# Kernel optimization log

Measured on AMD Instinct MI355X. Metric: run time of the kernel, lower is better.

## Reference

```python
import jax, jax.numpy as jnp
import numpy as np

N = 10000          # num nodes
E = 640000         # num edges (avg degree 64)
IN_CH = 128
OUT_CH = 128


def setup_inputs() -> dict:
    key = jax.random.key(0)
    k_x, k_ei, k_ea, k_w1, k_b1, k_w2, k_b2 = jax.random.split(key, 7)
    x = jax.random.normal(k_x, (N, IN_CH), dtype=jnp.float32)
    edge_index = jax.random.randint(k_ei, (2, E), 0, N, dtype=jnp.int64)
    edge_attr = jax.random.uniform(k_ea, (E,), dtype=jnp.float32)
    # MLP params: Linear(2*in, out) -> ReLU -> Linear(out, out), stored as [in, out]
    s1 = 1.0 / np.sqrt(2 * IN_CH)
    s2 = 1.0 / np.sqrt(OUT_CH)
    W1 = jax.random.uniform(k_w1, (2 * IN_CH, OUT_CH), jnp.float32, -s1, s1)
    b1 = jax.random.uniform(k_b1, (OUT_CH,), jnp.float32, -s1, s1)
    W2 = jax.random.uniform(k_w2, (OUT_CH, OUT_CH), jnp.float32, -s2, s2)
    b2 = jax.random.uniform(k_b2, (OUT_CH,), jnp.float32, -s2, s2)
    return {"x": x, "edge_index": edge_index, "edge_attr": edge_attr,
            "W1": W1, "b1": b1, "W2": W2, "b2": b2}


def reference(x, edge_index, edge_attr, W1, b1, W2, b2):
    row, col = edge_index[0], edge_index[1]
    # message: scale sender feature by edge_attr, concat with receiver feature, 2-layer MLP
    x_i = x[row] * edge_attr[:, None]          # [E, in]
    x_j = x[col]                               # [E, in]
    combined = jnp.concatenate([x_i, x_j], axis=1)  # [E, 2*in]
    h = jax.nn.relu(combined @ W1 + b1)        # [E, out]
    messages = h @ W2 + b2                     # [E, out]
    # sum aggregation: scatter-add messages into receiving nodes (col)
    out = jnp.zeros((x.shape[0], messages.shape[1]), dtype=messages.dtype)
    out = out.at[col].add(messages)
    return out
```

## Files before the change

kernel.cpp:

```cpp
#include <hip/hip_runtime.h>

#define C 128
#define NPB 16
#define NSLAB 8
#define CAP8 24
#define OVF_MAX 65536
#define EPT 8

__device__ __forceinline__ unsigned bf16_bits(float x) {
    unsigned u = __float_as_uint(x);
    u += 0x7FFFu + ((u >> 16) & 1u);
    return u >> 16;
}
__device__ __forceinline__ float bf16f(unsigned short b) {
    return __uint_as_float(((unsigned)b) << 16);
}

__global__ void fused_pre_kernel(const float* __restrict__ x, const float* __restrict__ W1,
                                 unsigned short* __restrict__ P16, float* __restrict__ Q,
                                 const int* __restrict__ ei, const float* __restrict__ attr,
                                 int* __restrict__ cursor, int* __restrict__ ovf_cnt,
                                 int2* __restrict__ ovf, unsigned* __restrict__ sorted,
                                 int N, int E, int SB) {
    if ((int)blockIdx.x < SB) {
        const int slab = blockIdx.x & (NSLAB - 1);
        int* __restrict__ cur = cursor + (size_t)slab * N;
        unsigned* __restrict__ sl = sorted + (size_t)slab * N * CAP8;
        const int base = (blockIdx.x * 256 + threadIdx.x) * EPT;
        if (base >= E) return;
        if (base + EPT <= E) {
            const int4 r0 = *(const int4*)(ei + base);
            const int4 r1 = *(const int4*)(ei + base + 4);
            const int4 c0 = *(const int4*)(ei + (size_t)E + base);
            const int4 c1 = *(const int4*)(ei + (size_t)E + base + 4);
            const float4 a0 = *(const float4*)(attr + base);
            const float4 a1 = *(const float4*)(attr + base + 4);
            const int rows[EPT] = {r0.x, r0.y, r0.z, r0.w, r1.x, r1.y, r1.z, r1.w};
            const int cols[EPT] = {c0.x, c0.y, c0.z, c0.w, c1.x, c1.y, c1.z, c1.w};
            const float as[EPT] = {a0.x, a0.y, a0.z, a0.w, a1.x, a1.y, a1.z, a1.w};
            int pos[EPT];
#pragma unroll
            for (int j = 0; j < EPT; ++j)
                pos[j] = atomicAdd(&cur[cols[j]], 1);
#pragma unroll
            for (int j = 0; j < EPT; ++j) {
                const unsigned v = (bf16_bits(as[j]) << 16) | (unsigned)rows[j];
                if (pos[j] < CAP8) {
                    sl[(size_t)cols[j] * CAP8 + pos[j]] = v;
                } else {
                    const int o = atomicAdd(ovf_cnt, 1);
                    if (o < OVF_MAX) ovf[o] = make_int2(cols[j], (int)v);
                }
            }
        } else {
            for (int e = base; e < E; ++e) {
                const int row = ei[e], colv = ei[(size_t)E + e];
                const int pos = atomicAdd(&cur[colv], 1);
                const unsigned v = (bf16_bits(attr[e]) << 16) | (unsigned)row;
                if (pos < CAP8) sl[(size_t)colv * CAP8 + pos] = v;
                else {
                    const int o = atomicAdd(ovf_cnt, 1);
                    if (o < OVF_MAX) ovf[o] = make_int2(colv, (int)v);
                }
            }
        }
    } else {
        __shared__ float xs[NPB][C];
        const int pb = blockIdx.x - SB;
        const int n0 = pb * NPB;
        const int tt = threadIdx.x & (C - 1);
        const int half = threadIdx.x >> 7;
        for (int i = threadIdx.x; i < NPB * C; i += 256) {
            const int gi = n0 * C + i;
            xs[0][i] = (gi < N * C) ? x[gi] : 0.f;
        }
        __syncthreads();
        const float* __restrict__ Wb = W1 + (half ? (C * C) : 0) + tt;
        float acc[NPB] = {};
        for (int k = 0; k < C; ++k) {
            const float w = Wb[k * C];
#pragma unroll
            for (int j = 0; j < NPB; ++j)
                acc[j] = fmaf(xs[j][k], w, acc[j]);
        }
#pragma unroll
        for (int j = 0; j < NPB; ++j)
            if (n0 + j < N) {
                if (half) Q[(size_t)(n0 + j) * C + tt] = acc[j];
                else      P16[(size_t)(n0 + j) * C + tt] = (unsigned short)bf16_bits(acc[j]);
            }
    }
}

__global__ void agg_out_kernel(const unsigned* __restrict__ sorted, const int* __restrict__ cursor,
                               const unsigned short* __restrict__ P16, const float* __restrict__ Q,
                               const float* __restrict__ b1, const float* __restrict__ W2,
                               const float* __restrict__ b2,
                               const int* __restrict__ ovf_cnt, const int2* __restrict__ ovf,
                               float* __restrict__ out, int N) {
    __shared__ float4 part[2][4][32];
    __shared__ float hs[2][C];
    const int t = threadIdx.x;
    const int j = t >> 7;
    const int slice = (t >> 5) & 3;
    const int ch4 = t & 31;
    const int n = blockIdx.x * 2 + j;

    float4 acc = make_float4(0.f, 0.f, 0.f, 0.f);
    float4 qb = acc;
    int deg = 0;
    if (n < N) {
        int cnts[NSLAB];
#pragma unroll
        for (int s = 0; s < NSLAB; ++s) {
            cnts[s] = cursor[(size_t)s * N + n];
            deg += cnts[s];
        }
        const float4 q4  = *(const float4*)(Q + (size_t)n * C + (ch4 << 2));
        const float4 b14 = *(const float4*)(b1 + (ch4 << 2));
        qb = make_float4(q4.x + b14.x, q4.y + b14.y, q4.z + b14.z, q4.w + b14.w);
#pragma unroll
        for (int si = 0; si < 2; ++si) {
            const int s = slice + (si << 2);
            const int cs = min(cnts[s], CAP8);
            const unsigned* __restrict__ buf = sorted + ((size_t)s * N + n) * CAP8;
            int i = 0;
            for (; i + 4 <= cs; i += 4) {
                const uint4 v = *(const uint4*)(buf + i);
                const ushort4 p0 = *(const ushort4*)(P16 + (((size_t)(v.x & 0xFFFFu)) << 7) + (ch4 << 2));
                const ushort4 p1 = *(const ushort4*)(P16 + (((size_t)(v.y & 0xFFFFu)) << 7) + (ch4 << 2));
                const ushort4 p2 = *(const ushort4*)(P16 + (((size_t)(v.z & 0xFFFFu)) << 7) + (ch4 << 2));
                const ushort4 p3 = *(const ushort4*)(P16 + (((size_t)(v.w & 0xFFFFu)) << 7) + (ch4 << 2));
                const float a0 = __uint_as_float(v.x & 0xFFFF0000u);
                const float a1 = __uint_as_float(v.y & 0xFFFF0000u);
                const float a2 = __uint_as_float(v.z & 0xFFFF0000u);
                const float a3 = __uint_as_float(v.w & 0xFFFF0000u);
                acc.x += fmaxf(fmaf(a0, bf16f(p0.x), qb.x), 0.f) + fmaxf(fmaf(a1, bf16f(p1.x), qb.x), 0.f)
                       + fmaxf(fmaf(a2, bf16f(p2.x), qb.x), 0.f) + fmaxf(fmaf(a3, bf16f(p3.x), qb.x), 0.f);
                acc.y += fmaxf(fmaf(a0, bf16f(p0.y), qb.y), 0.f) + fmaxf(fmaf(a1, bf16f(p1.y), qb.y), 0.f)
                       + fmaxf(fmaf(a2, bf16f(p2.y), qb.y), 0.f) + fmaxf(fmaf(a3, bf16f(p3.y), qb.y), 0.f);
                acc.z += fmaxf(fmaf(a0, bf16f(p0.z), qb.z), 0.f) + fmaxf(fmaf(a1, bf16f(p1.z), qb.z), 0.f)
                       + fmaxf(fmaf(a2, bf16f(p2.z), qb.z), 0.f) + fmaxf(fmaf(a3, bf16f(p3.z), qb.z), 0.f);
                acc.w += fmaxf(fmaf(a0, bf16f(p0.w), qb.w), 0.f) + fmaxf(fmaf(a1, bf16f(p1.w), qb.w), 0.f)
                       + fmaxf(fmaf(a2, bf16f(p2.w), qb.w), 0.f) + fmaxf(fmaf(a3, bf16f(p3.w), qb.w), 0.f);
            }
            for (; i < cs; ++i) {
                const unsigned v = buf[i];
                const ushort4 p = *(const ushort4*)(P16 + (((size_t)(v & 0xFFFFu)) << 7) + (ch4 << 2));
                const float a = __uint_as_float(v & 0xFFFF0000u);
                acc.x += fmaxf(fmaf(a, bf16f(p.x), qb.x), 0.f);
                acc.y += fmaxf(fmaf(a, bf16f(p.y), qb.y), 0.f);
                acc.z += fmaxf(fmaf(a, bf16f(p.z), qb.z), 0.f);
                acc.w += fmaxf(fmaf(a, bf16f(p.w), qb.w), 0.f);
            }
        }
        if (slice == 0) {
            const int oc = min(*ovf_cnt, OVF_MAX);
            for (int o = 0; o < oc; ++o) {
                const int2 v = ovf[o];
                if (v.x == n) {
                    const unsigned u = (unsigned)v.y;
                    const ushort4 p = *(const ushort4*)(P16 + (((size_t)(u & 0xFFFFu)) << 7) + (ch4 << 2));
                    const float a = __uint_as_float(u & 0xFFFF0000u);
                    acc.x += fmaxf(fmaf(a, bf16f(p.x), qb.x), 0.f);
                    acc.y += fmaxf(fmaf(a, bf16f(p.y), qb.y), 0.f);
                    acc.z += fmaxf(fmaf(a, bf16f(p.z), qb.z), 0.f);
                    acc.w += fmaxf(fmaf(a, bf16f(p.w), qb.w), 0.f);
                }
            }
        }
    }
    part[j][slice][ch4] = acc;
    __syncthreads();
    if (slice == 0 && n < N) {
        const float4 r0 = part[j][0][ch4], r1 = part[j][1][ch4];
        const float4 r2 = part[j][2][ch4], r3 = part[j][3][ch4];
        float4 h;
        h.x = r0.x + r1.x + r2.x + r3.x;
        h.y = r0.y + r1.y + r2.y + r3.y;
        h.z = r0.z + r1.z + r2.z + r3.z;
        h.w = r0.w + r1.w + r2.w + r3.w;
        *(float4*)(&hs[j][ch4 << 2]) = h;
    }
    __syncthreads();
    float4 o = make_float4(0.f, 0.f, 0.f, 0.f);
    if (n < N) {
        const int k0 = slice << 5;
#pragma unroll 8
        for (int k = k0; k < k0 + 32; ++k) {
            const float hv = hs[j][k];
            const float4 w = *(const float4*)(W2 + (size_t)k * C + (ch4 << 2));
            o.x = fmaf(hv, w.x, o.x);
            o.y = fmaf(hv, w.y, o.y);
            o.z = fmaf(hv, w.z, o.z);
            o.w = fmaf(hv, w.w, o.w);
        }
    }
    __syncthreads();
    part[j][slice][ch4] = o;
    __syncthreads();
    if (slice == 0 && n < N) {
        const float4 r0 = part[j][0][ch4], r1 = part[j][1][ch4];
        const float4 r2 = part[j][2][ch4], r3 = part[j][3][ch4];
        const float4 b24 = *(const float4*)(b2 + (ch4 << 2));
        const float d = (float)deg;
        float4 res;
        res.x = fmaf(d, b24.x, r0.x + r1.x + r2.x + r3.x);
        res.y = fmaf(d, b24.y, r0.y + r1.y + r2.y + r3.y);
        res.z = fmaf(d, b24.z, r0.z + r1.z + r2.z + r3.z);
        res.w = fmaf(d, b24.w, r0.w + r1.w + r2.w + r3.w);
        *(float4*)(out + (size_t)n * C + (ch4 << 2)) = res;
    }
}

extern "C" void kernel_launch(void* const* d_in, const int* in_sizes, int n_in,
                              void* d_out, int out_size, void* d_ws, size_t ws_size,
                              hipStream_t stream) {
    const float* x    = (const float*)d_in[0];
    const int*   ei   = (const int*)d_in[1];
    const float* attr = (const float*)d_in[2];
    const float* W1   = (const float*)d_in[3];
    const float* b1   = (const float*)d_in[4];
    const float* W2   = (const float*)d_in[5];
    const float* b2   = (const float*)d_in[6];
    float* out = (float*)d_out;

    const int N = in_sizes[0] / C;
    const int E = in_sizes[2];

    char* ws = (char*)d_ws;
    unsigned short* P16 = (unsigned short*)ws;  ws += (size_t)N * C * sizeof(unsigned short);
    ws = (char*)(((uintptr_t)ws + 15) & ~(uintptr_t)15);
    float*    Q       = (float*)ws;     ws += (size_t)N * C * sizeof(float);
    unsigned* sorted  = (unsigned*)ws;  ws += (size_t)NSLAB * N * CAP8 * sizeof(unsigned);
    int2*     ovf     = (int2*)ws;      ws += (size_t)OVF_MAX * sizeof(int2);
    int*      cursor  = (int*)ws;       ws += (size_t)NSLAB * N * sizeof(int);
    int*      ovf_cnt = (int*)ws;

    hipMemsetAsync(cursor, 0, ((size_t)NSLAB * N + 1) * sizeof(int), stream);

    const int SB = (E + 256 * EPT - 1) / (256 * EPT);
    const int PB = (N + NPB - 1) / NPB;
    fused_pre_kernel<<<SB + PB, 256, 0, stream>>>(x, W1, P16, Q, ei, attr,
                                                  cursor, ovf_cnt, ovf, sorted, N, E, SB);
    agg_out_kernel<<<(N + 1) / 2, 256, 0, stream>>>(sorted, cursor, P16, Q, b1, W2, b2,
                                                    ovf_cnt, ovf, out, N);
}
```

Measured before the change: 159.2 us.

## Pick bucket slab by XCD, shrink bucket capacity, interleave two-slab gather loop

The bucketing phase now chooses the cursor/sorted slab from the hardware XCD id, so atomics to each slab stay local to one XCD's L2. Per-slab bucket capacity drops from 24 to 16 entries so indexing becomes a shift, each thread handles 4 edges instead of 8, and input loads use nontemporal hints. The aggregation loop interleaves two slabs so eight gathers are in flight per iteration. Smaller capacity may push more edges to the overflow list, which every node's thread scans linearly. That scan risks extra cost, and the slab can become uneven if the XCD assignment is skewed.

New measurement: 267.2 us. +67.8%, slower.

```diff
diff --git a/kernel.cpp b/kernel.cpp
--- a/kernel.cpp
+++ b/kernel.cpp
@@ -3,9 +3,12 @@
 #define C 128
 #define NPB 16
 #define NSLAB 8
-#define CAP8 24
+#define CAP8 16
 #define OVF_MAX 65536
-#define EPT 8
+#define EPT 4
+
+typedef int   vi4 __attribute__((ext_vector_type(4)));
+typedef float vf4 __attribute__((ext_vector_type(4)));
 
 __device__ __forceinline__ unsigned bf16_bits(float x) {
     unsigned u = __float_as_uint(x);
@@ -14,6 +17,9 @@
 }
 __device__ __forceinline__ float bf16f(unsigned short b) {
     return __uint_as_float(((unsigned)b) << 16);
+}
+__device__ __forceinline__ int xcd_id() {
+    return (int)(__builtin_amdgcn_s_getreg(63508) & 7u);
 }
 
 __global__ void fused_pre_kernel(const float* __restrict__ x, const float* __restrict__ W1,
@@ -23,21 +29,18 @@
                                  int2* __restrict__ ovf, unsigned* __restrict__ sorted,
                                  int N, int E, int SB) {
     if ((int)blockIdx.x < SB) {
-        const int slab = blockIdx.x & (NSLAB - 1);
+        const int slab = xcd_id();
         int* __restrict__ cur = cursor + (size_t)slab * N;
-        unsigned* __restrict__ sl = sorted + (size_t)slab * N * CAP8;
+        unsigned* __restrict__ sl = sorted + ((size_t)slab * N) * CAP8;
         const int base = (blockIdx.x * 256 + threadIdx.x) * EPT;
         if (base >= E) return;
         if (base + EPT <= E) {
-            const int4 r0 = *(const int4*)(ei + base);
-            const int4 r1 = *(const int4*)(ei + base + 4);
-            const int4 c0 = *(const int4*)(ei + (size_t)E + base);
-            const int4 c1 = *(const int4*)(ei + (size_t)E + base + 4);
-            const float4 a0 = *(const float4*)(attr + base);
-            const float4 a1 = *(const float4*)(attr + base + 4);
-            const int rows[EPT] = {r0.x, r0.y, r0.z, r0.w, r1.x, r1.y, r1.z, r1.w};
-            const int cols[EPT] = {c0.x, c0.y, c0.z, c0.w, c1.x, c1.y, c1.z, c1.w};
-            const float as[EPT] = {a0.x, a0.y, a0.z, a0.w, a1.x, a1.y, a1.z, a1.w};
+            const vi4 r0 = __builtin_nontemporal_load((const vi4*)(ei + base));
+            const vi4 c0 = __builtin_nontemporal_load((const vi4*)(ei + (size_t)E + base));
+            const vf4 a0 = __builtin_nontemporal_load((const vf4*)(attr + base));
+            const int rows[EPT] = {r0.x, r0.y, r0.z, r0.w};
+            const int cols[EPT] = {c0.x, c0.y, c0.z, c0.w};
+            const float as[EPT] = {a0.x, a0.y, a0.z, a0.w};
             int pos[EPT];
 #pragma unroll
             for (int j = 0; j < EPT; ++j)
@@ -46,7 +49,7 @@
             for (int j = 0; j < EPT; ++j) {
                 const unsigned v = (bf16_bits(as[j]) << 16) | (unsigned)rows[j];
                 if (pos[j] < CAP8) {
-                    sl[(size_t)cols[j] * CAP8 + pos[j]] = v;
+                    sl[((size_t)cols[j] << 4) + pos[j]] = v;
                 } else {
                     const int o = atomicAdd(ovf_cnt, 1);
                     if (o < OVF_MAX) ovf[o] = make_int2(cols[j], (int)v);
@@ -57,7 +60,7 @@
                 const int row = ei[e], colv = ei[(size_t)E + e];
                 const int pos = atomicAdd(&cur[colv], 1);
                 const unsigned v = (bf16_bits(attr[e]) << 16) | (unsigned)row;
-                if (pos < CAP8) sl[(size_t)colv * CAP8 + pos] = v;
+                if (pos < CAP8) sl[((size_t)colv << 4) + pos] = v;
                 else {
                     const int o = atomicAdd(ovf_cnt, 1);
                     if (o < OVF_MAX) ovf[o] = make_int2(colv, (int)v);
@@ -72,7 +75,7 @@
         const int half = threadIdx.x >> 7;
         for (int i = threadIdx.x; i < NPB * C; i += 256) {
             const int gi = n0 * C + i;
-            xs[0][i] = (gi < N * C) ? x[gi] : 0.f;
+            xs[0][i] = (gi < N * C) ? __builtin_nontemporal_load(x + gi) : 0.f;
         }
         __syncthreads();
         const float* __restrict__ Wb = W1 + (half ? (C * C) : 0) + tt;
@@ -90,6 +93,20 @@
                 else      P16[(size_t)(n0 + j) * C + tt] = (unsigned short)bf16_bits(acc[j]);
             }
     }
+}
+
+struct G { ushort4 p; float a; };
+__device__ __forceinline__ G gat(unsigned v, const unsigned short* __restrict__ P16, int ch4) {
+    G g;
+    g.p = *(const ushort4*)(P16 + (((size_t)(v & 0xFFFFu)) << 7) + (ch4 << 2));
+    g.a = __uint_as_float(v & 0xFFFF0000u);
+    return g;
+}
+__device__ __forceinline__ void upd(float4& acc, const G& g, const float4& qb) {
+    acc.x += fmaxf(fmaf(g.a, bf16f(g.p.x), qb.x), 0.f);
+    acc.y += fmaxf(fmaf(g.a, bf16f(g.p.y), qb.y), 0.f);
+    acc.z += fmaxf(fmaf(g.a, bf16f(g.p.z), qb.z), 0.f);
+    acc.w += fmaxf(fmaf(g.a, bf16f(g.p.w), qb.w), 0.f);
 }
 
 __global__ void agg_out_kernel(const unsigned* __restrict__ sorted, const int* __restrict__ cursor,
@@ -119,54 +136,43 @@
         const float4 q4  = *(const float4*)(Q + (size_t)n * C + (ch4 << 2));
         const float4 b14 = *(const float4*)(b1 + (ch4 << 2));
         qb = make_float4(q4.x + b14.x, q4.y + b14.y, q4.z + b14.z, q4.w + b14.w);
-#pragma unroll
-        for (int si = 0; si < 2; ++si) {
-            const int s = slice + (si << 2);
-            const int cs = min(cnts[s], CAP8);
-            const unsigned* __restrict__ buf = sorted + ((size_t)s * N + n) * CAP8;
-            int i = 0;
-            for (; i + 4 <= cs; i += 4) {
-                const uint4 v = *(const uint4*)(buf + i);
-                const ushort4 p0 = *(const ushort4*)(P16 + (((size_t)(v.x & 0xFFFFu)) << 7) + (ch4 << 2));
-                const ushort4 p1 = *(const ushort4*)(P16 + (((size_t)(v.y & 0xFFFFu)) << 7) + (ch4 << 2));
-                const ushort4 p2 = *(const ushort4*)(P16 + (((size_t)(v.z & 0xFFFFu)) << 7) + (ch4 << 2));
-                const ushort4 p3 = *(const ushort4*)(P16 + (((size_t)(v.w & 0xFFFFu)) << 7) + (ch4 << 2));
-                const float a0 = __uint_as_float(v.x & 0xFFFF0000u);
-                const float a1 = __uint_as_float(v.y & 0xFFFF0000u);
-                const float a2 = __uint_as_float(v.z & 0xFFFF0000u);
-                const float a3 = __uint_as_float(v.w & 0xFFFF0000u);
-                acc.x += fmaxf(fmaf(a0, bf16f(p0.x), qb.x), 0.f) + fmaxf(fmaf(a1, bf16f(p1.x), qb.x), 0.f)
-                       + fmaxf(fmaf(a2, bf16f(p2.x), qb.x), 0.f) + fmaxf(fmaf(a3, bf16f(p3.x), qb.x), 0.f);
-                acc.y += fmaxf(fmaf(a0, bf16f(p0.y), qb.y), 0.f) + fmaxf(fmaf(a1, bf16f(p1.y), qb.y), 0.f)
-                       + fmaxf(fmaf(a2, bf16f(p2.y), qb.y), 0.f) + fmaxf(fmaf(a3, bf16f(p3.y), qb.y), 0.f);
-                acc.z += fmaxf(fmaf(a0, bf16f(p0.z), qb.z), 0.f) + fmaxf(fmaf(a1, bf16f(p1.z), qb.z), 0.f)
-                       + fmaxf(fmaf(a2, bf16f(p2.z), qb.z), 0.f) + fmaxf(fmaf(a3, bf16f(p3.z), qb.z), 0.f);
-                acc.w += fmaxf(fmaf(a0, bf16f(p0.w), qb.w), 0.f) + fmaxf(fmaf(a1, bf16f(p1.w), qb.w), 0.f)
-                       + fmaxf(fmaf(a2, bf16f(p2.w), qb.w), 0.f) + fmaxf(fmaf(a3, bf16f(p3.w), qb.w), 0.f);
-            }
-            for (; i < cs; ++i) {
-                const unsigned v = buf[i];
-                const ushort4 p = *(const ushort4*)(P16 + (((size_t)(v & 0xFFFFu)) << 7) + (ch4 << 2));
-                const float a = __uint_as_float(v & 0xFFFF0000u);
-                acc.x += fmaxf(fmaf(a, bf16f(p.x), qb.x), 0.f);
-                acc.y += fmaxf(fmaf(a, bf16f(p.y), qb.y), 0.f);
-                acc.z += fmaxf(fmaf(a, bf16f(p.z), qb.z), 0.f);
-                acc.w += fmaxf(fmaf(a, bf16f(p.w), qb.w), 0.f);
-            }
-        }
+
+        const int sA = slice, sB = slice + 4;
+        const int cA = min(cnts[sA], CAP8), cB = min(cnts[sB], CAP8);
+        const unsigned* __restrict__ bufA = sorted + (((size_t)sA * N + n) << 4);
+        const unsigned* __restrict__ bufB = sorted + (((size_t)sB * N + n) << 4);
+        int iA = 0, iB = 0;
+        while (iA + 4 <= cA && iB + 4 <= cB) {
+            const uint4 vA = *(const uint4*)(bufA + iA);
+            const uint4 vB = *(const uint4*)(bufB + iB);
+            const G g0 = gat(vA.x, P16, ch4), g1 = gat(vA.y, P16, ch4);
+            const G g2 = gat(vA.z, P16, ch4), g3 = gat(vA.w, P16, ch4);
+            const G g4 = gat(vB.x, P16, ch4), g5 = gat(vB.y, P16, ch4);
+            const G g6 = gat(vB.z, P16, ch4), g7 = gat(vB.w, P16, ch4);
+            upd(acc, g0, qb); upd(acc, g1, qb); upd(acc, g2, qb); upd(acc, g3, qb);
+            upd(acc, g4, qb); upd(acc, g5, qb); upd(acc, g6, qb); upd(acc, g7, qb);
+            iA += 4; iB += 4;
+        }
+        for (; iA + 4 <= cA; iA += 4) {
+            const uint4 v = *(const uint4*)(bufA + iA);
+            const G g0 = gat(v.x, P16, ch4), g1 = gat(v.y, P16, ch4);
+            const G g2 = gat(v.z, P16, ch4), g3 = gat(v.w, P16, ch4);
+            upd(acc, g0, qb); upd(acc, g1, qb); upd(acc, g2, qb); upd(acc, g3, qb);
+        }
+        for (; iB + 4 <= cB; iB += 4) {
+            const uint4 v = *(const uint4*)(bufB + iB);
+            const G g0 = gat(v.x, P16, ch4), g1 = gat(v.y, P16, ch4);
+            const G g2 = gat(v.z, P16, ch4), g3 = gat(v.w, P16, ch4);
+            upd(acc, g0, qb); upd(acc, g1, qb); upd(acc, g2, qb); upd(acc, g3, qb);
+        }
+        for (; iA < cA; ++iA) { const G g = gat(bufA[iA], P16, ch4); upd(acc, g, qb); }
+        for (; iB < cB; ++iB) { const G g = gat(bufB[iB], P16, ch4); upd(acc, g, qb); }
+
         if (slice == 0) {
             const int oc = min(*ovf_cnt, OVF_MAX);
             for (int o = 0; o < oc; ++o) {
                 const int2 v = ovf[o];
-                if (v.x == n) {
-                    const unsigned u = (unsigned)v.y;
-                    const ushort4 p = *(const ushort4*)(P16 + (((size_t)(u & 0xFFFFu)) << 7) + (ch4 << 2));
-                    const float a = __uint_as_float(u & 0xFFFF0000u);
-                    acc.x += fmaxf(fmaf(a, bf16f(p.x), qb.x), 0.f);
-                    acc.y += fmaxf(fmaf(a, bf16f(p.y), qb.y), 0.f);
-                    acc.z += fmaxf(fmaf(a, bf16f(p.z), qb.z), 0.f);
-                    acc.w += fmaxf(fmaf(a, bf16f(p.w), qb.w), 0.f);
-                }
+                if (v.x == n) { const G g = gat((unsigned)v.y, P16, ch4); upd(acc, g, qb); }
             }
         }
     }
@@ -237,7 +243,7 @@
     int*      cursor  = (int*)ws;       ws += (size_t)NSLAB * N * sizeof(int);
     int*      ovf_cnt = (int*)ws;
 
-    hipMemsetAsync(cursor, 0, ((size_t)NSLAB * N + 1) * sizeof(int), stream);
+    (void)hipMemsetAsync(cursor, 0, ((size_t)NSLAB * N + 1) * sizeof(int), stream);
 
     const int SB = (E + 256 * EPT - 1) / (256 * EPT);
     const int PB = (N + NPB - 1) / NPB;
```
